# Kernel tuning notes

Hardware: AMD Instinct MI355X
Metric: run time of the kernel (lower is better)

## Reference

```python
import jax, jax.numpy as jnp
import numpy as np
from jax.scipy.linalg import solve_triangular

B, T, S, L, R, H = 64, 100, 32, 128, 16, 256

def bmv(A, v):
    return jnp.einsum('...ij,...j->...i', A, v)

def mT(A):
    return jnp.swapaxes(A, -1, -2)

def tri_inv_mT(chol):
    # Psi = inv(chol).T (upper triangular); chol is batched lower-triangular
    r = chol.shape[-1]
    I = jnp.broadcast_to(jnp.eye(r, dtype=chol.dtype), chol.shape)
    return mT(solve_triangular(chol, I, lower=True))

def chol_bmv_solve(Psi, v):
    # (chol chol^T)^{-1} v, using Psi = inv(chol)^T -> A^{-1} = Psi Psi^T
    return bmv(Psi, bmv(mT(Psi), v))

def filter_step_0(m_0, k0, K0, P_p_diag, w_p, w_f):
    # K0: (B,L,R); w_p: (S,B,L); w_f: (S,B,R)
    r = K0.shape[-1]
    z_p_c = jnp.sqrt(P_p_diag) * w_p
    m_p = jnp.broadcast_to(m_0, K0.shape[:1] + m_0.shape)  # (B,L)
    h = (1.0 / P_p_diag) * m_p + k0
    P_p_K = P_p_diag[None, :, None] * K0                    # (B,L,R)
    M = jnp.eye(r, dtype=K0.dtype) + mT(K0) @ P_p_K
    Psi = tri_inv_mT(jnp.linalg.cholesky(M))
    m = P_p_diag * h - bmv(P_p_K, chol_bmv_solve(Psi, bmv(mT(P_p_K), h)))
    v_1 = bmv(mT(K0), z_p_c) + w_f
    z = m + z_p_c - bmv(K0, chol_bmv_solve(Psi, v_1))
    return z, m

def predict_step(m_theta, Q_diag, w1, w2):
    # m_theta: (B,L,S) dynamics-mean particles
    s = m_theta.shape[-1]
    m_p = m_theta.mean(-1)                                   # (B,L)
    M_c = (m_theta - m_p[..., None]) * (1.0 / np.sqrt(s))    # (B,L,S)
    McT_Qinv = mT(M_c) * (1.0 / Q_diag)
    Psi_p = tri_inv_mT(jnp.linalg.cholesky(jnp.eye(s, dtype=m_theta.dtype) + McT_Qinv @ M_c))
    u1 = m_p / Q_diag
    u2 = (1.0 / Q_diag) * bmv(M_c, bmv(Psi_p, bmv(mT(Psi_p), bmv(mT(M_c), u1))))
    h_p = u1 - u2                                            # P_p^{-1} m_p (Woodbury)
    z_p_c = bmv(M_c, w1) + jnp.sqrt(Q_diag) * w2             # (S,B,L)
    return z_p_c, m_p, h_p, M_c

def update_step(z_p_c, h_p, k_t, K_t, w_f, M_c_p, Q_diag):
    r = K_t.shape[-1]
    Q_sqrt = jnp.sqrt(Q_diag)
    h = h_p + k_t
    K_M = mT(K_t) @ M_c_p                                    # (B,R,S)
    K_Q = mT(K_t) * Q_sqrt
    KPK = K_M @ mT(K_M) + K_Q @ mT(K_Q)                      # K^T P_p K
    Psi = tri_inv_mT(jnp.linalg.cholesky(jnp.eye(r, dtype=K_t.dtype) + KPK))
    P_p = lambda v: bmv(M_c_p, bmv(mT(M_c_p), v)) + Q_diag * v
    u1 = P_p(h)
    trip = bmv(K_t, bmv(Psi, bmv(mT(Psi), bmv(mT(K_t), u1))))
    m = u1 - P_p(trip)                                       # P_f h via Woodbury
    v_1 = bmv(mT(K_t), z_p_c) + w_f
    z = m + z_p_c - bmv(K_t, chol_bmv_solve(Psi, v_1))
    return m, z

def forward(k, K, m_0, P_p_diag, Q_diag, W1, W2, w_p0, w_f0, w_p1_seq, w_p2_seq, w_f_seq):
    mean_fn = lambda z: z + jnp.tanh(z @ W1) @ W2            # nonlinear dynamics mean
    k_tm = jnp.moveaxis(k, 1, 0)                              # (T,B,L)
    K_tm = jnp.moveaxis(K, 1, 0)                              # (T,B,L,R)
    z0, _ = filter_step_0(m_0, k_tm[0], K_tm[0], P_p_diag, w_p0, w_f0)

    def step(z_prev, inp):
        kt, Kt, w1, w2, wf = inp
        m_theta = jnp.moveaxis(mean_fn(z_prev), 0, -1)        # (B,L,S)
        z_p_c, m_p, h_p, M_c = predict_step(m_theta, Q_diag, w1, w2)
        m_f, z_f = update_step(z_p_c, h_p, kt, Kt, wf, M_c, Q_diag)
        return z_f, z_f

    _, zs = jax.lax.scan(step, z0, (k_tm[1:], K_tm[1:], w_p1_seq, w_p2_seq, w_f_seq))
    return jnp.concatenate([z0[None], zs], axis=0)            # (T,S,B,L)

def setup_inputs() -> dict:
    key = jax.random.key(0)
    ks = jax.random.split(key, 12)
    return {
        'k': 0.5 * jax.random.normal(ks[0], (B, T, L), jnp.float32),
        'K': 0.2 * jax.random.normal(ks[1], (B, T, L, R), jnp.float32),
        'm_0': jax.random.normal(ks[2], (L,), jnp.float32),
        'P_p_diag': jax.random.uniform(ks[3], (L,), jnp.float32, 0.5, 1.5),
        'Q_diag': jax.random.uniform(ks[4], (L,), jnp.float32, 0.5, 1.5),
        'W1': 0.02 * jax.random.normal(ks[5], (L, H), jnp.float32),
        'W2': 0.02 * jax.random.normal(ks[6], (H, L), jnp.float32),
        'w_p0': jax.random.normal(ks[7], (S, B, L), jnp.float32),
        'w_f0': jax.random.normal(ks[8], (S, B, R), jnp.float32),
        'w_p1_seq': jax.random.normal(ks[9], (T - 1, S, B, S), jnp.float32),
        'w_p2_seq': jax.random.normal(ks[10], (T - 1, S, B, L), jnp.float32),
        'w_f_seq': jax.random.normal(ks[11], (T - 1, S, B, R), jnp.float32),
    }

def reference(k, K, m_0, P_p_diag, Q_diag, W1, W2, w_p0, w_f0, w_p1_seq, w_p2_seq, w_f_seq):
    return forward(k, K, m_0, P_p_diag, Q_diag, W1, W2, w_p0, w_f0, w_p1_seq, w_p2_seq, w_f_seq)
```

## Files before the change

kernel.cpp:

```cpp
#include <hip/hip_runtime.h>
#include <math.h>

#define B_ 64
#define T_ 100
#define S_ 32
#define L_ 128
#define R_ 16
#define H_ 256

__device__ __forceinline__ float dot4(float4 a, float4 b) {
  return a.x*b.x + a.y*b.y + a.z*b.z + a.w*b.w;
}
__device__ __forceinline__ void wave_fence() {
  asm volatile("s_waitcnt lgkmcnt(0)" ::: "memory");
  __builtin_amdgcn_wave_barrier();
}

__device__ __forceinline__ void chol16_inv(int lane, float (*C2)[17], float (*G)[17], float* rd) {
  float row[16];
  #pragma unroll
  for (int c = 0; c < 16; ++c) row[c] = (lane < 16) ? C2[lane][c] : 0.0f;
  float rdg = 0.0f;
  #pragma unroll
  for (int j = 0; j < 16; ++j) {
    float dsq = __shfl(row[j], j);
    float d = sqrtf(dsq);
    float inv = 1.0f / d;
    float cij = row[j] * inv;
    if (lane == j) { cij = d; rdg = inv; }
    row[j] = cij;
    float upd = (lane > j) ? (cij * inv) : 0.0f;
    #pragma unroll
    for (int c = j + 1; c < 16; ++c) {
      float cjc = __shfl(row[c], j);
      row[c] -= upd * cjc;
    }
  }
  if (lane < 16) {
    #pragma unroll
    for (int c = 0; c < 16; ++c) C2[lane][c] = row[c];
    rd[lane] = rdg;
  }
  wave_fence();
  if (lane < 16) {
    const int c = lane;
    float g[16];
    #pragma unroll
    for (int i = 0; i < 16; ++i) {
      float a = (i == c) ? 1.0f : 0.0f;
      #pragma unroll
      for (int j2 = 0; j2 < 16; ++j2) if (j2 < i) a -= C2[i][j2] * g[j2];
      g[i] = a * rd[i];
    }
    #pragma unroll
    for (int i = 0; i < 16; ++i) G[i][c] = (i >= c) ? g[i] : 0.0f;
  }
  wave_fence();
}

__device__ __forceinline__ void chol32_solve(int lane, float (*C)[33], float* rd32,
                                             const float* t1, float* xb) {
  float row[32];
  #pragma unroll
  for (int c = 0; c < 32; ++c) row[c] = (lane < 32) ? C[lane][c] : 0.0f;
  float rdg = 0.0f;
  #pragma unroll
  for (int j = 0; j < 32; ++j) {
    float dsq = __shfl(row[j], j);
    float d = sqrtf(dsq);
    float inv = 1.0f / d;
    float cij = row[j] * inv;
    if (lane == j) { cij = d; rdg = inv; }
    row[j] = cij;
    float upd = (lane > j) ? (cij * inv) : 0.0f;
    #pragma unroll
    for (int c = j + 1; c < 32; ++c) {
      float cjc = __shfl(row[c], j);
      row[c] -= upd * cjc;
    }
  }
  float acc = (lane < 32) ? t1[lane] : 0.0f;
  #pragma unroll
  for (int j = 0; j < 32; ++j) {
    float xj = __shfl(acc, j) * __shfl(rdg, j);
    if (lane == j) acc = xj;
    else if (lane > j) acc -= row[j] * xj;
  }
  if (lane < 32) {
    #pragma unroll
    for (int c = 0; c < 32; ++c) C[lane][c] = row[c];
    rd32[lane] = rdg;
  }
  wave_fence();
  float acc2 = acc;
  #pragma unroll
  for (int j = 31; j >= 0; --j) {
    if (lane == j) xb[j] = acc2 * rdg;
    wave_fence();
    float xj = xb[j];
    if (lane < j) acc2 -= C[j][lane] * xj;
  }
}

__global__ __launch_bounds__(512) void filter_kernel(
    const float* __restrict__ kg,
    const float* __restrict__ Kg,
    const float* __restrict__ m0g,
    const float* __restrict__ Ppg,
    const float* __restrict__ Qg,
    const float* __restrict__ wp0,
    const float* __restrict__ wf0,
    const float* __restrict__ wp1s,
    const float* __restrict__ wp2s,
    const float* __restrict__ wfs,
    const float* __restrict__ W1,
    const float* __restrict__ W2,
    float* __restrict__ out)
{
  const int b = blockIdx.x;
  const int tid = threadIdx.x;

  __shared__ float zc[S_][132];
  __shared__ float Ab[S_][264];
  __shared__ float Mc[S_][132];
  __shared__ float zp[S_][132];
  __shared__ float KtT[R_][132];
  __shared__ float w1b[S_][36];
  __shared__ float wfb[S_][20];
  __shared__ float C32m[32][33];
  __shared__ float C2m[16][17];
  __shared__ float Gm[16][17];
  __shared__ float KMm[16][36];
  __shared__ float v1b[S_][20];
  __shared__ float yb[S_][20];
  __shared__ float xv[S_][20];
  __shared__ float red[32][17];
  __shared__ float mp[L_], u1[L_], hv[L_], uu[L_], mv[L_], trp[L_], ktv[L_];
  __shared__ float Qv[L_], iQ[L_], sQ[L_], Ppv[L_], sPp[L_], m0v[L_];
  __shared__ float t1v[32], tPh[32], xbuf[32], rd32[32];
  __shared__ float ttv[16], ssv[16], rd16[16], y2v[16];

  if (tid < L_) {
    float q = Qg[tid];  Qv[tid] = q;  iQ[tid] = 1.0f / q;  sQ[tid] = sqrtf(q);
    float p = Ppg[tid]; Ppv[tid] = p; sPp[tid] = sqrtf(p);
    m0v[tid] = m0g[tid];
  }
  __syncthreads();

  {
    {
      const float* Ksrc = Kg + (size_t)b * T_ * L_ * R_;
      float4 v = *(const float4*)(Ksrc + tid * 4);
      int l = (tid * 4) >> 4, r = (tid * 4) & 15;
      KtT[r+0][l] = v.x; KtT[r+1][l] = v.y; KtT[r+2][l] = v.z; KtT[r+3][l] = v.w;
    }
    for (int e = tid; e < S_ * L_ / 4; e += 512) {
      int s = e >> 5, l = (e & 31) * 4;
      float4 w = *(const float4*)(wp0 + ((size_t)s * B_ + b) * L_ + l);
      float4 p = *(const float4*)&sPp[l];
      *(float4*)&zp[s][l] = make_float4(w.x*p.x, w.y*p.y, w.z*p.z, w.w*p.w);
    }
    { int s = tid >> 4, r = tid & 15;
      wfb[s][r] = wf0[((size_t)s * B_ + b) * R_ + r]; }
    __syncthreads();

    if (tid < 256) {
      int r1 = tid >> 4, r2 = tid & 15;
      if (r1 <= r2) {
        float acc = (r1 == r2) ? 1.0f : 0.0f;
        for (int lc = 0; lc < 32; ++lc) {
          float4 a = *(const float4*)&KtT[r1][lc*4];
          float4 c = *(const float4*)&KtT[r2][lc*4];
          float4 p = *(const float4*)&Ppv[lc*4];
          acc += a.x*c.x*p.x + a.y*c.y*p.y + a.z*c.z*p.z + a.w*c.w*p.w;
        }
        C2m[r1][r2] = acc; C2m[r2][r1] = acc;
      }
      if (tid < 128) hv[tid] = m0v[tid] / Ppv[tid] + kg[(size_t)b * T_ * L_ + tid];
    } else {
      int q2 = tid - 256, s = q2 >> 3, r = (q2 & 7) * 2;
      float a0 = wfb[s][r], a1 = wfb[s][r+1];
      for (int lc = 0; lc < 32; ++lc) {
        float4 zz = *(const float4*)&zp[s][lc*4];
        float4 ka = *(const float4*)&KtT[r][lc*4];
        float4 kb = *(const float4*)&KtT[r+1][lc*4];
        a0 += dot4(zz, ka); a1 += dot4(zz, kb);
      }
      v1b[s][r] = a0; v1b[s][r+1] = a1;
    }
    __syncthreads();
    if (tid < 64) chol16_inv(tid, C2m, Gm, rd16);
    __syncthreads();
    {
      int r = tid & 15, g = tid >> 4;
      float4 a = *(const float4*)&KtT[r][g*4];
      float4 p = *(const float4*)&Ppv[g*4];
      float4 h4 = *(const float4*)&hv[g*4];
      red[g][r] = a.x*p.x*h4.x + a.y*p.y*h4.y + a.z*p.z*h4.z + a.w*p.w*h4.w;
    }
    { int s = tid >> 4, r = tid & 15;
      float a = 0;
      #pragma unroll
      for (int j = 0; j < 16; ++j) a += Gm[r][j] * v1b[s][j];
      yb[s][r] = a; }
    __syncthreads();
    {
      int s = tid >> 4, r = tid & 15;
      float a = 0;
      #pragma unroll
      for (int j = 0; j < 16; ++j) a += Gm[j][r] * yb[s][j];
      xv[s][r] = a; }
    if (tid < 64) {
      if (tid < 16) { float a = 0;
        #pragma unroll
        for (int g = 0; g < 32; ++g) a += red[g][tid];
        ttv[tid] = a; }
      wave_fence();
      if (tid < 16) { float a = 0;
        #pragma unroll
        for (int j = 0; j < 16; ++j) a += Gm[tid][j] * ttv[j];
        y2v[tid] = a; }
      wave_fence();
      if (tid < 16) { float a = 0;
        #pragma unroll
        for (int j = 0; j < 16; ++j) a += Gm[j][tid] * y2v[j];
        ssv[tid] = a; }
    }
    __syncthreads();
    if (tid < 128) {
      float a = hv[tid];
      #pragma unroll
      for (int r = 0; r < 16; ++r) a -= KtT[r][tid] * ssv[r];
      mv[tid] = Ppv[tid] * a;
    }
    __syncthreads();
    {
      int s = tid >> 4, l0 = (tid & 15) * 8;
      float acc[8] = {0,0,0,0,0,0,0,0};
      #pragma unroll
      for (int r = 0; r < 16; ++r) {
        float xr = xv[s][r];
        float4 k1 = *(const float4*)&KtT[r][l0];
        float4 k2 = *(const float4*)&KtT[r][l0+4];
        acc[0] += k1.x*xr; acc[1] += k1.y*xr; acc[2] += k1.z*xr; acc[3] += k1.w*xr;
        acc[4] += k2.x*xr; acc[5] += k2.y*xr; acc[6] += k2.z*xr; acc[7] += k2.w*xr;
      }
      float4 o1, o2;
      o1.x = mv[l0+0] + zp[s][l0+0] - acc[0]; o1.y = mv[l0+1] + zp[s][l0+1] - acc[1];
      o1.z = mv[l0+2] + zp[s][l0+2] - acc[2]; o1.w = mv[l0+3] + zp[s][l0+3] - acc[3];
      o2.x = mv[l0+4] + zp[s][l0+4] - acc[4]; o2.y = mv[l0+5] + zp[s][l0+5] - acc[5];
      o2.z = mv[l0+6] + zp[s][l0+6] - acc[6]; o2.w = mv[l0+7] + zp[s][l0+7] - acc[7];
      *(float4*)&zc[s][l0] = o1; *(float4*)&zc[s][l0+4] = o2;
      float* orow = out + ((size_t)s * B_ + b) * L_ + l0;
      *(float4*)orow = o1; *(float4*)(orow + 4) = o2;
    }
    __syncthreads();
  }

  for (int t = 1; t < T_; ++t) {
    {
      const float* Ksrc = Kg + ((size_t)b * T_ + t) * L_ * R_;
      float4 v = *(const float4*)(Ksrc + tid * 4);
      int l = (tid * 4) >> 4, r = (tid * 4) & 15;
      KtT[r+0][l] = v.x; KtT[r+1][l] = v.y; KtT[r+2][l] = v.z; KtT[r+3][l] = v.w;
    }
    if (tid < 128) ktv[tid] = kg[((size_t)b * T_ + t) * L_ + tid];
    { int s = tid >> 4, r = tid & 15;
      wfb[s][r] = wfs[(((size_t)(t-1) * S_ + s) * B_ + b) * R_ + r]; }
    { int e = tid * 2, s = e >> 5, j = e & 31;
      float2 v = *(const float2*)(wp1s + (((size_t)(t-1) * S_ + s) * B_ + b) * S_ + j);
      w1b[s][j] = v.x; w1b[s][j+1] = v.y; }

    {
      int s = tid & 31, h0 = (tid >> 5) * 16;
      float acc[16] = {0,0,0,0,0,0,0,0,0,0,0,0,0,0,0,0};
      for (int lc = 0; lc < 32; ++lc) {
        float4 z4 = *(const float4*)&zc[s][lc*4];
        float zv[4] = {z4.x, z4.y, z4.z, z4.w};
        #pragma unroll
        for (int q = 0; q < 4; ++q) {
          const float* wrow = W1 + (lc*4 + q) * H_ + h0;
          float4 wa = *(const float4*)(wrow);
          float4 wb = *(const float4*)(wrow + 4);
          float4 wc = *(const float4*)(wrow + 8);
          float4 wd = *(const float4*)(wrow + 12);
          float zq = zv[q];
          acc[0]  += zq*wa.x; acc[1]  += zq*wa.y; acc[2]  += zq*wa.z; acc[3]  += zq*wa.w;
          acc[4]  += zq*wb.x; acc[5]  += zq*wb.y; acc[6]  += zq*wb.z; acc[7]  += zq*wb.w;
          acc[8]  += zq*wc.x; acc[9]  += zq*wc.y; acc[10] += zq*wc.z; acc[11] += zq*wc.w;
          acc[12] += zq*wd.x; acc[13] += zq*wd.y; acc[14] += zq*wd.z; acc[15] += zq*wd.w;
        }
      }
      #pragma unroll
      for (int j = 0; j < 16; ++j) Ab[s][h0 + j] = tanhf(acc[j]);
    }
    __syncthreads();
    {
      int s = tid & 31, l0 = (tid >> 5) * 8;
      float acc[8] = {0,0,0,0,0,0,0,0};
      for (int hc = 0; hc < 64; ++hc) {
        float4 a4 = *(const float4*)&Ab[s][hc*4];
        float av[4] = {a4.x, a4.y, a4.z, a4.w};
        #pragma unroll
        for (int q = 0; q < 4; ++q) {
          const float* wrow = W2 + (hc*4 + q) * L_ + l0;
          float4 wa = *(const float4*)(wrow);
          float4 wb = *(const float4*)(wrow + 4);
          float aq = av[q];
          acc[0] += aq*wa.x; acc[1] += aq*wa.y; acc[2] += aq*wa.z; acc[3] += aq*wa.w;
          acc[4] += aq*wb.x; acc[5] += aq*wb.y; acc[6] += aq*wb.z; acc[7] += aq*wb.w;
        }
      }
      #pragma unroll
      for (int j = 0; j < 8; ++j) Mc[s][l0 + j] = zc[s][l0 + j] + acc[j];
    }
    __syncthreads();
    if (tid < 128) {
      float m = 0;
      #pragma unroll 8
      for (int s = 0; s < 32; ++s) m += Mc[s][tid];
      m *= (1.0f / 32.0f);
      mp[tid] = m; u1[tid] = m * iQ[tid];
    }
    __syncthreads();
    for (int e = tid; e < S_ * L_; e += 512) {
      int s = e >> 7, l = e & 127;
      float v = (Mc[s][l] - mp[l]) * 0.17677669529663687f;
      Mc[s][l] = v; Ab[s][l] = v * iQ[l];
    }
    __syncthreads();
    for (int e = tid; e < 1024; e += 512) {
      int s1 = e >> 5, s2 = e & 31;
      if (s1 <= s2) {
        float acc = (s1 == s2) ? 1.0f : 0.0f;
        for (int lc = 0; lc < 32; ++lc) {
          float4 a = *(const float4*)&Ab[s1][lc*4];
          float4 c = *(const float4*)&Mc[s2][lc*4];
          acc += dot4(a, c);
        }
        C32m[s1][s2] = acc; C32m[s2][s1] = acc;
      }
    }
    { int s = tid >> 4, r = tid & 15;
      float acc = 0;
      for (int lc = 0; lc < 32; ++lc) {
        float4 kk = *(const float4*)&KtT[r][lc*4];
        float4 mm = *(const float4*)&Mc[s][lc*4];
        acc += dot4(kk, mm);
      }
      KMm[r][s] = acc; }
    { int s = tid >> 4, g = tid & 15, l0 = g * 8;
      float4 m1 = *(const float4*)&Mc[s][l0];
      float4 m2 = *(const float4*)&Mc[s][l0+4];
      float4 a1 = *(const float4*)&u1[l0];
      float4 a2 = *(const float4*)&u1[l0+4];
      red[s][g] = dot4(m1, a1) + dot4(m2, a2); }
    { int s = tid >> 4, l0 = (tid & 15) * 8;
      float acc[8] = {0,0,0,0,0,0,0,0};
      for (int j = 0; j < 32; ++j) {
        float wj = w1b[s][j];
        float4 m1 = *(const float4*)&Mc[j][l0];
        float4 m2 = *(const float4*)&Mc[j][l0+4];
        acc[0] += m1.x*wj; acc[1] += m1.y*wj; acc[2] += m1.z*wj; acc[3] += m1.w*wj;
        acc[4] += m2.x*wj; acc[5] += m2.y*wj; acc[6] += m2.z*wj; acc[7] += m2.w*wj;
      }
      const float* w2src = wp2s + (((size_t)(t-1) * S_ + s) * B_ + b) * L_ + l0;
      float4 wa = *(const float4*)(w2src);
      float4 wb2 = *(const float4*)(w2src + 4);
      float4 q1 = *(const float4*)&sQ[l0];
      float4 q2 = *(const float4*)&sQ[l0+4];
      *(float4*)&zp[s][l0]   = make_float4(acc[0]+q1.x*wa.x,  acc[1]+q1.y*wa.y,
                                           acc[2]+q1.z*wa.z,  acc[3]+q1.w*wa.w);
      *(float4*)&zp[s][l0+4] = make_float4(acc[4]+q2.x*wb2.x, acc[5]+q2.y*wb2.y,
                                           acc[6]+q2.z*wb2.z, acc[7]+q2.w*wb2.w); }
    __syncthreads();
    if (tid < 256) {
      int r1 = tid >> 4, r2 = tid & 15;
      if (r1 <= r2) {
        float acc = (r1 == r2) ? 1.0f : 0.0f;
        #pragma unroll
        for (int sc2 = 0; sc2 < 8; ++sc2) {
          float4 a = *(const float4*)&KMm[r1][sc2*4];
          float4 c = *(const float4*)&KMm[r2][sc2*4];
          acc += dot4(a, c);
        }
        for (int lc = 0; lc < 32; ++lc) {
          float4 a = *(const float4*)&KtT[r1][lc*4];
          float4 c = *(const float4*)&KtT[r2][lc*4];
          float4 q = *(const float4*)&Qv[lc*4];
          acc += a.x*c.x*q.x + a.y*c.y*q.y + a.z*c.z*q.z + a.w*c.w*q.w;
        }
        C2m[r1][r2] = acc; C2m[r2][r1] = acc;
      }
      if (tid < 32) { float a = 0;
        #pragma unroll
        for (int g = 0; g < 16; ++g) a += red[tid][g];
        t1v[tid] = a; }
    } else {
      int q2 = tid - 256, s = q2 >> 3, r = (q2 & 7) * 2;
      float a0 = wfb[s][r], a1 = wfb[s][r+1];
      for (int lc = 0; lc < 32; ++lc) {
        float4 zz = *(const float4*)&zp[s][lc*4];
        float4 ka = *(const float4*)&KtT[r][lc*4];
        float4 kb = *(const float4*)&KtT[r+1][lc*4];
        a0 += dot4(zz, ka); a1 += dot4(zz, kb);
      }
      v1b[s][r] = a0; v1b[s][r+1] = a1;
    }
    __syncthreads();
    if (tid < 64) chol32_solve(tid, C32m, rd32, t1v, xbuf);
    else if (tid < 128) chol16_inv(tid - 64, C2m, Gm, rd16);
    __syncthreads();
    { int s = tid >> 4, r = tid & 15;
      float a = 0;
      #pragma unroll
      for (int j = 0; j < 16; ++j) a += Gm[r][j] * v1b[s][j];
      yb[s][r] = a; }
    if (tid < 128) {
      float a = u1[tid];
      #pragma unroll 8
      for (int s = 0; s < 32; ++s) a -= Ab[s][tid] * xbuf[s];
      hv[tid] = a + ktv[tid];
    }
    __syncthreads();
    { int s = tid >> 4, r = tid & 15;
      float a = 0;
      #pragma unroll
      for (int j = 0; j < 16; ++j) a += Gm[j][r] * yb[s][j];
      xv[s][r] = a; }
    { int s = tid >> 4, g = tid & 15, l0 = g * 8;
      float4 m1 = *(const float4*)&Mc[s][l0];
      float4 m2 = *(const float4*)&Mc[s][l0+4];
      float4 h1 = *(const float4*)&hv[l0];
      float4 h2 = *(const float4*)&hv[l0+4];
      red[s][g] = dot4(m1, h1) + dot4(m2, h2); }
    __syncthreads();
    if (tid < 32) { float a = 0;
      #pragma unroll
      for (int g = 0; g < 16; ++g) a += red[tid][g];
      tPh[tid] = a; }
    __syncthreads();
    if (tid < 128) {
      float a = Qv[tid] * hv[tid];
      #pragma unroll 8
      for (int s = 0; s < 32; ++s) a += Mc[s][tid] * tPh[s];
      uu[tid] = a;
    }
    __syncthreads();
    { int r = tid & 15, g = tid >> 4;
      float4 a = *(const float4*)&KtT[r][g*4];
      float4 u4 = *(const float4*)&uu[g*4];
      red[g][r] = dot4(a, u4); }
    __syncthreads();
    if (tid < 64) {
      if (tid < 16) { float a = 0;
        #pragma unroll
        for (int g = 0; g < 32; ++g) a += red[g][tid];
        ttv[tid] = a; }
      wave_fence();
      if (tid < 16) { float a = 0;
        #pragma unroll
        for (int j = 0; j < 16; ++j) a += Gm[tid][j] * ttv[j];
        y2v[tid] = a; }
      wave_fence();
      if (tid < 16) { float a = 0;
        #pragma unroll
        for (int j = 0; j < 16; ++j) a += Gm[j][tid] * y2v[j];
        ssv[tid] = a; }
    }
    __syncthreads();
    if (tid < 128) {
      float a = 0;
      #pragma unroll
      for (int r = 0; r < 16; ++r) a += KtT[r][tid] * ssv[r];
      trp[tid] = a;
    }
    __syncthreads();
    { int s = tid >> 4, g = tid & 15, l0 = g * 8;
      float4 m1 = *(const float4*)&Mc[s][l0];
      float4 m2 = *(const float4*)&Mc[s][l0+4];
      float4 h1 = *(const float4*)&trp[l0];
      float4 h2 = *(const float4*)&trp[l0+4];
      red[s][g] = dot4(m1, h1) + dot4(m2, h2); }
    __syncthreads();
    if (tid < 32) { float a = 0;
      #pragma unroll
      for (int g = 0; g < 16; ++g) a += red[tid][g];
      tPh[tid] = a; }
    __syncthreads();
    if (tid < 128) {
      float a = uu[tid] - Qv[tid] * trp[tid];
      #pragma unroll 8
      for (int s = 0; s < 32; ++s) a -= Mc[s][tid] * tPh[s];
      mv[tid] = a;
    }
    __syncthreads();
    {
      int s = tid >> 4, l0 = (tid & 15) * 8;
      float acc[8] = {0,0,0,0,0,0,0,0};
      #pragma unroll
      for (int r = 0; r < 16; ++r) {
        float xr = xv[s][r];
        float4 k1 = *(const float4*)&KtT[r][l0];
        float4 k2 = *(const float4*)&KtT[r][l0+4];
        acc[0] += k1.x*xr; acc[1] += k1.y*xr; acc[2] += k1.z*xr; acc[3] += k1.w*xr;
        acc[4] += k2.x*xr; acc[5] += k2.y*xr; acc[6] += k2.z*xr; acc[7] += k2.w*xr;
      }
      float4 o1, o2;
      o1.x = mv[l0+0] + zp[s][l0+0] - acc[0]; o1.y = mv[l0+1] + zp[s][l0+1] - acc[1];
      o1.z = mv[l0+2] + zp[s][l0+2] - acc[2]; o1.w = mv[l0+3] + zp[s][l0+3] - acc[3];
      o2.x = mv[l0+4] + zp[s][l0+4] - acc[4]; o2.y = mv[l0+5] + zp[s][l0+5] - acc[5];
      o2.z = mv[l0+6] + zp[s][l0+6] - acc[6]; o2.w = mv[l0+7] + zp[s][l0+7] - acc[7];
      *(float4*)&zc[s][l0] = o1; *(float4*)&zc[s][l0+4] = o2;
      float* orow = out + (((size_t)t * S_ + s) * B_ + b) * L_ + l0;
      *(float4*)orow = o1; *(float4*)(orow + 4) = o2;
    }
    __syncthreads();
  }
}

extern "C" void kernel_launch(void* const* d_in, const int* in_sizes, int n_in,
                              void* d_out, int out_size, void* d_ws, size_t ws_size,
                              hipStream_t stream) {
  const float* kg  = (const float*)d_in[0];
  const float* Kg  = (const float*)d_in[1];
  const float* m0  = (const float*)d_in[2];
  const float* Pp  = (const float*)d_in[3];
  const float* Qd  = (const float*)d_in[4];
  const float* W1  = (const float*)d_in[5];
  const float* W2  = (const float*)d_in[6];
  const float* wp0 = (const float*)d_in[7];
  const float* wf0 = (const float*)d_in[8];
  const float* wp1 = (const float*)d_in[9];
  const float* wp2 = (const float*)d_in[10];
  const float* wfs = (const float*)d_in[11];
  float* outp = (float*)d_out;
  (void)d_ws; (void)ws_size;

  filter_kernel<<<B_, 512, 0, stream>>>(kg, Kg, m0, Pp, Qd, wp0, wf0,
                                        wp1, wp2, wfs, W1, W2, outp);
}
```

Baseline: 8.575 ms.

## Double block to 1024 threads and collapse serial update chain into one wave

Each block now runs 1024 threads. The MLP and prediction phases are re-split so each thread does less work. The long chain of small reductions in the update step (hv, tPh, uu, ttv, ssv, trp, mv), which used many block-wide barriers, now runs inside a single 64-lane wave using shuffles and wave fences, while other waves compute the Kalman-gain correction to zp in parallel. The 32x32 back-substitution now uses register shuffles instead of per-step LDS writes and fences, and a transposed Mc copy is added for column access. The aim is to cut __syncthreads count and latency on this serial per-timestep path. The cost is more LDS use, more register pressure under the 1024-thread launch bound, and most threads sitting idle during the single-wave section.

```diff
diff --git a/kernel.cpp b/kernel.cpp
--- a/kernel.cpp
+++ b/kernel.cpp
@@ -58,8 +58,8 @@
   wave_fence();
 }
 
-__device__ __forceinline__ void chol32_solve(int lane, float (*C)[33], float* rd32,
-                                             const float* t1, float* xb) {
+__device__ __forceinline__ void chol32_fs(int lane, float (*C)[33],
+                                          const float* t1, float* xb) {
   float row[32];
   #pragma unroll
   for (int c = 0; c < 32; ++c) row[c] = (lane < 32) ? C[lane][c] : 0.0f;
@@ -89,20 +89,24 @@
   if (lane < 32) {
     #pragma unroll
     for (int c = 0; c < 32; ++c) C[lane][c] = row[c];
-    rd32[lane] = rdg;
   }
   wave_fence();
+  float colT[32];
+  #pragma unroll
+  for (int j = 0; j < 32; ++j) colT[j] = (lane < 32) ? C[j][lane] : 0.0f;
   float acc2 = acc;
+  float xi = 0.0f;
   #pragma unroll
   for (int j = 31; j >= 0; --j) {
-    if (lane == j) xb[j] = acc2 * rdg;
-    wave_fence();
-    float xj = xb[j];
-    if (lane < j) acc2 -= C[j][lane] * xj;
-  }
+    float xj = __shfl(acc2, j) * __shfl(rdg, j);
+    if (lane == j) xi = xj;
+    if (lane < j) acc2 -= colT[j] * xj;
+  }
+  if (lane < 32) xb[lane] = xi;
+  wave_fence();
 }
 
-__global__ __launch_bounds__(512) void filter_kernel(
+__global__ __launch_bounds__(1024) void filter_kernel(
     const float* __restrict__ kg,
     const float* __restrict__ Kg,
     const float* __restrict__ m0g,
@@ -123,6 +127,7 @@
   __shared__ float zc[S_][132];
   __shared__ float Ab[S_][264];
   __shared__ float Mc[S_][132];
+  __shared__ float McT[L_][33];
   __shared__ float zp[S_][132];
   __shared__ float KtT[R_][132];
   __shared__ float w1b[S_][36];
@@ -133,11 +138,11 @@
   __shared__ float KMm[16][36];
   __shared__ float v1b[S_][20];
   __shared__ float yb[S_][20];
-  __shared__ float xv[S_][20];
+  __shared__ float xvb[S_][20];
   __shared__ float red[32][17];
   __shared__ float mp[L_], u1[L_], hv[L_], uu[L_], mv[L_], trp[L_], ktv[L_];
   __shared__ float Qv[L_], iQ[L_], sQ[L_], Ppv[L_], sPp[L_], m0v[L_];
-  __shared__ float t1v[32], tPh[32], xbuf[32], rd32[32];
+  __shared__ float t1v[32], tPh[32], xbuf[32];
   __shared__ float ttv[16], ssv[16], rd16[16], y2v[16];
 
   if (tid < L_) {
@@ -148,19 +153,19 @@
   __syncthreads();
 
   {
-    {
+    if (tid < 512) {
       const float* Ksrc = Kg + (size_t)b * T_ * L_ * R_;
       float4 v = *(const float4*)(Ksrc + tid * 4);
       int l = (tid * 4) >> 4, r = (tid * 4) & 15;
       KtT[r+0][l] = v.x; KtT[r+1][l] = v.y; KtT[r+2][l] = v.z; KtT[r+3][l] = v.w;
     }
-    for (int e = tid; e < S_ * L_ / 4; e += 512) {
-      int s = e >> 5, l = (e & 31) * 4;
+    {
+      int s = tid >> 5, l = (tid & 31) * 4;
       float4 w = *(const float4*)(wp0 + ((size_t)s * B_ + b) * L_ + l);
       float4 p = *(const float4*)&sPp[l];
       *(float4*)&zp[s][l] = make_float4(w.x*p.x, w.y*p.y, w.z*p.z, w.w*p.w);
     }
-    { int s = tid >> 4, r = tid & 15;
+    if (tid < 512) { int s = tid >> 4, r = tid & 15;
       wfb[s][r] = wf0[((size_t)s * B_ + b) * R_ + r]; }
     __syncthreads();
 
@@ -177,7 +182,7 @@
         C2m[r1][r2] = acc; C2m[r2][r1] = acc;
       }
       if (tid < 128) hv[tid] = m0v[tid] / Ppv[tid] + kg[(size_t)b * T_ * L_ + tid];
-    } else {
+    } else if (tid < 512) {
       int q2 = tid - 256, s = q2 >> 3, r = (q2 & 7) * 2;
       float a0 = wfb[s][r], a1 = wfb[s][r+1];
       for (int lc = 0; lc < 32; ++lc) {
@@ -191,25 +196,24 @@
     __syncthreads();
     if (tid < 64) chol16_inv(tid, C2m, Gm, rd16);
     __syncthreads();
-    {
-      int r = tid & 15, g = tid >> 4;
-      float4 a = *(const float4*)&KtT[r][g*4];
-      float4 p = *(const float4*)&Ppv[g*4];
-      float4 h4 = *(const float4*)&hv[g*4];
-      red[g][r] = a.x*p.x*h4.x + a.y*p.y*h4.y + a.z*p.z*h4.z + a.w*p.w*h4.w;
-    }
-    { int s = tid >> 4, r = tid & 15;
+    if (tid < 512) {
+      { int r = tid & 15, g = tid >> 4;
+        float4 a = *(const float4*)&KtT[r][g*4];
+        float4 p = *(const float4*)&Ppv[g*4];
+        float4 h4 = *(const float4*)&hv[g*4];
+        red[g][r] = a.x*p.x*h4.x + a.y*p.y*h4.y + a.z*p.z*h4.z + a.w*p.w*h4.w; }
+      { int s = tid >> 4, r = tid & 15;
+        float a = 0;
+        #pragma unroll
+        for (int j = 0; j < 16; ++j) a += Gm[r][j] * v1b[s][j];
+        yb[s][r] = a; }
+    }
+    __syncthreads();
+    if (tid < 512) { int s = tid >> 4, r = tid & 15;
       float a = 0;
       #pragma unroll
-      for (int j = 0; j < 16; ++j) a += Gm[r][j] * v1b[s][j];
-      yb[s][r] = a; }
-    __syncthreads();
-    {
-      int s = tid >> 4, r = tid & 15;
-      float a = 0;
-      #pragma unroll
       for (int j = 0; j < 16; ++j) a += Gm[j][r] * yb[s][j];
-      xv[s][r] = a; }
+      xvb[s][r] = a; }
     if (tid < 64) {
       if (tid < 16) { float a = 0;
         #pragma unroll
@@ -234,12 +238,12 @@
       mv[tid] = Ppv[tid] * a;
     }
     __syncthreads();
-    {
+    if (tid < 512) {
       int s = tid >> 4, l0 = (tid & 15) * 8;
       float acc[8] = {0,0,0,0,0,0,0,0};
       #pragma unroll
       for (int r = 0; r < 16; ++r) {
-        float xr = xv[s][r];
+        float xr = xvb[s][r];
         float4 k1 = *(const float4*)&KtT[r][l0];
         float4 k2 = *(const float4*)&KtT[r][l0+4];
         acc[0] += k1.x*xr; acc[1] += k1.y*xr; acc[2] += k1.z*xr; acc[3] += k1.w*xr;
@@ -258,61 +262,56 @@
   }
 
   for (int t = 1; t < T_; ++t) {
-    {
+    if (tid < 512) {
       const float* Ksrc = Kg + ((size_t)b * T_ + t) * L_ * R_;
       float4 v = *(const float4*)(Ksrc + tid * 4);
       int l = (tid * 4) >> 4, r = (tid * 4) & 15;
       KtT[r+0][l] = v.x; KtT[r+1][l] = v.y; KtT[r+2][l] = v.z; KtT[r+3][l] = v.w;
-    }
-    if (tid < 128) ktv[tid] = kg[((size_t)b * T_ + t) * L_ + tid];
-    { int s = tid >> 4, r = tid & 15;
-      wfb[s][r] = wfs[(((size_t)(t-1) * S_ + s) * B_ + b) * R_ + r]; }
-    { int e = tid * 2, s = e >> 5, j = e & 31;
+      int s = tid >> 4, rr = tid & 15;
+      wfb[s][rr] = wfs[(((size_t)(t-1) * S_ + s) * B_ + b) * R_ + rr];
+      if (tid < 128) ktv[tid] = kg[((size_t)b * T_ + t) * L_ + tid];
+    } else {
+      int e = (tid - 512) * 2, s = e >> 5, j = e & 31;
       float2 v = *(const float2*)(wp1s + (((size_t)(t-1) * S_ + s) * B_ + b) * S_ + j);
-      w1b[s][j] = v.x; w1b[s][j+1] = v.y; }
+      w1b[s][j] = v.x; w1b[s][j+1] = v.y;
+    }
 
     {
-      int s = tid & 31, h0 = (tid >> 5) * 16;
-      float acc[16] = {0,0,0,0,0,0,0,0,0,0,0,0,0,0,0,0};
+      int s = tid >> 5, h0 = (tid & 31) * 8;
+      float acc[8] = {0,0,0,0,0,0,0,0};
       for (int lc = 0; lc < 32; ++lc) {
         float4 z4 = *(const float4*)&zc[s][lc*4];
+        const float* wbase = W1 + (size_t)(lc*4) * H_ + h0;
         float zv[4] = {z4.x, z4.y, z4.z, z4.w};
         #pragma unroll
         for (int q = 0; q < 4; ++q) {
-          const float* wrow = W1 + (lc*4 + q) * H_ + h0;
-          float4 wa = *(const float4*)(wrow);
-          float4 wb = *(const float4*)(wrow + 4);
-          float4 wc = *(const float4*)(wrow + 8);
-          float4 wd = *(const float4*)(wrow + 12);
+          float4 wa = *(const float4*)(wbase + q*H_);
+          float4 wb = *(const float4*)(wbase + q*H_ + 4);
           float zq = zv[q];
-          acc[0]  += zq*wa.x; acc[1]  += zq*wa.y; acc[2]  += zq*wa.z; acc[3]  += zq*wa.w;
-          acc[4]  += zq*wb.x; acc[5]  += zq*wb.y; acc[6]  += zq*wb.z; acc[7]  += zq*wb.w;
-          acc[8]  += zq*wc.x; acc[9]  += zq*wc.y; acc[10] += zq*wc.z; acc[11] += zq*wc.w;
-          acc[12] += zq*wd.x; acc[13] += zq*wd.y; acc[14] += zq*wd.z; acc[15] += zq*wd.w;
-        }
-      }
-      #pragma unroll
-      for (int j = 0; j < 16; ++j) Ab[s][h0 + j] = tanhf(acc[j]);
+          acc[0] += zq*wa.x; acc[1] += zq*wa.y; acc[2] += zq*wa.z; acc[3] += zq*wa.w;
+          acc[4] += zq*wb.x; acc[5] += zq*wb.y; acc[6] += zq*wb.z; acc[7] += zq*wb.w;
+        }
+      }
+      #pragma unroll
+      for (int j = 0; j < 8; ++j) Ab[s][h0 + j] = tanhf(acc[j]);
     }
     __syncthreads();
     {
-      int s = tid & 31, l0 = (tid >> 5) * 8;
-      float acc[8] = {0,0,0,0,0,0,0,0};
+      int s = tid >> 5, l0 = (tid & 31) * 4;
+      float acc[4] = {0,0,0,0};
       for (int hc = 0; hc < 64; ++hc) {
         float4 a4 = *(const float4*)&Ab[s][hc*4];
+        const float* wbase = W2 + (size_t)(hc*4) * L_ + l0;
         float av[4] = {a4.x, a4.y, a4.z, a4.w};
         #pragma unroll
         for (int q = 0; q < 4; ++q) {
-          const float* wrow = W2 + (hc*4 + q) * L_ + l0;
-          float4 wa = *(const float4*)(wrow);
-          float4 wb = *(const float4*)(wrow + 4);
+          float4 w = *(const float4*)(wbase + q*L_);
           float aq = av[q];
-          acc[0] += aq*wa.x; acc[1] += aq*wa.y; acc[2] += aq*wa.z; acc[3] += aq*wa.w;
-          acc[4] += aq*wb.x; acc[5] += aq*wb.y; acc[6] += aq*wb.z; acc[7] += aq*wb.w;
-        }
-      }
-      #pragma unroll
-      for (int j = 0; j < 8; ++j) Mc[s][l0 + j] = zc[s][l0 + j] + acc[j];
+          acc[0] += aq*w.x; acc[1] += aq*w.y; acc[2] += aq*w.z; acc[3] += aq*w.w;
+        }
+      }
+      float4 z4 = *(const float4*)&zc[s][l0];
+      *(float4*)&Mc[s][l0] = make_float4(z4.x+acc[0], z4.y+acc[1], z4.z+acc[2], z4.w+acc[3]);
     }
     __syncthreads();
     if (tid < 128) {
@@ -323,56 +322,58 @@
       mp[tid] = m; u1[tid] = m * iQ[tid];
     }
     __syncthreads();
-    for (int e = tid; e < S_ * L_; e += 512) {
-      int s = e >> 7, l = e & 127;
-      float v = (Mc[s][l] - mp[l]) * 0.17677669529663687f;
-      Mc[s][l] = v; Ab[s][l] = v * iQ[l];
-    }
-    __syncthreads();
-    for (int e = tid; e < 1024; e += 512) {
-      int s1 = e >> 5, s2 = e & 31;
-      if (s1 <= s2) {
-        float acc = (s1 == s2) ? 1.0f : 0.0f;
+    {
+      int s = tid >> 5, l0 = (tid & 31) * 4;
+      float4 m4 = *(const float4*)&Mc[s][l0];
+      float4 p4 = *(const float4*)&mp[l0];
+      float4 q4 = *(const float4*)&iQ[l0];
+      const float cs = 0.17677669529663687f;
+      float4 v4 = make_float4((m4.x-p4.x)*cs, (m4.y-p4.y)*cs, (m4.z-p4.z)*cs, (m4.w-p4.w)*cs);
+      *(float4*)&Mc[s][l0] = v4;
+      *(float4*)&Ab[s][l0] = make_float4(v4.x*q4.x, v4.y*q4.y, v4.z*q4.z, v4.w*q4.w);
+      McT[l0+0][s] = v4.x; McT[l0+1][s] = v4.y; McT[l0+2][s] = v4.z; McT[l0+3][s] = v4.w;
+    }
+    __syncthreads();
+    {
+      { int s1 = tid >> 5, s2 = tid & 31;
+        if (s1 <= s2) {
+          float acc = (s1 == s2) ? 1.0f : 0.0f;
+          for (int lc = 0; lc < 32; ++lc) {
+            float4 a = *(const float4*)&Ab[s1][lc*4];
+            float4 c = *(const float4*)&Mc[s2][lc*4];
+            acc += dot4(a, c);
+          }
+          C32m[s1][s2] = acc; C32m[s2][s1] = acc;
+        } }
+      if (tid < 512) { int r = tid >> 5, s = tid & 31;
+        float acc = 0;
         for (int lc = 0; lc < 32; ++lc) {
-          float4 a = *(const float4*)&Ab[s1][lc*4];
-          float4 c = *(const float4*)&Mc[s2][lc*4];
-          acc += dot4(a, c);
-        }
-        C32m[s1][s2] = acc; C32m[s2][s1] = acc;
-      }
-    }
-    { int s = tid >> 4, r = tid & 15;
-      float acc = 0;
-      for (int lc = 0; lc < 32; ++lc) {
-        float4 kk = *(const float4*)&KtT[r][lc*4];
-        float4 mm = *(const float4*)&Mc[s][lc*4];
-        acc += dot4(kk, mm);
-      }
-      KMm[r][s] = acc; }
-    { int s = tid >> 4, g = tid & 15, l0 = g * 8;
-      float4 m1 = *(const float4*)&Mc[s][l0];
-      float4 m2 = *(const float4*)&Mc[s][l0+4];
-      float4 a1 = *(const float4*)&u1[l0];
-      float4 a2 = *(const float4*)&u1[l0+4];
-      red[s][g] = dot4(m1, a1) + dot4(m2, a2); }
-    { int s = tid >> 4, l0 = (tid & 15) * 8;
-      float acc[8] = {0,0,0,0,0,0,0,0};
-      for (int j = 0; j < 32; ++j) {
-        float wj = w1b[s][j];
-        float4 m1 = *(const float4*)&Mc[j][l0];
-        float4 m2 = *(const float4*)&Mc[j][l0+4];
-        acc[0] += m1.x*wj; acc[1] += m1.y*wj; acc[2] += m1.z*wj; acc[3] += m1.w*wj;
-        acc[4] += m2.x*wj; acc[5] += m2.y*wj; acc[6] += m2.z*wj; acc[7] += m2.w*wj;
-      }
-      const float* w2src = wp2s + (((size_t)(t-1) * S_ + s) * B_ + b) * L_ + l0;
-      float4 wa = *(const float4*)(w2src);
-      float4 wb2 = *(const float4*)(w2src + 4);
-      float4 q1 = *(const float4*)&sQ[l0];
-      float4 q2 = *(const float4*)&sQ[l0+4];
-      *(float4*)&zp[s][l0]   = make_float4(acc[0]+q1.x*wa.x,  acc[1]+q1.y*wa.y,
-                                           acc[2]+q1.z*wa.z,  acc[3]+q1.w*wa.w);
-      *(float4*)&zp[s][l0+4] = make_float4(acc[4]+q2.x*wb2.x, acc[5]+q2.y*wb2.y,
-                                           acc[6]+q2.z*wb2.z, acc[7]+q2.w*wb2.w); }
+          float4 kk = *(const float4*)&KtT[r][lc*4];
+          float4 mm = *(const float4*)&Mc[s][lc*4];
+          acc += dot4(kk, mm);
+        }
+        KMm[r][s] = acc;
+      } else { int g = tid - 512, s = g >> 4, seg = g & 15;
+        float4 m1 = *(const float4*)&Mc[s][seg*8];
+        float4 m2 = *(const float4*)&Mc[s][seg*8+4];
+        float4 a1 = *(const float4*)&u1[seg*8];
+        float4 a2 = *(const float4*)&u1[seg*8+4];
+        red[s][seg] = dot4(m1, a1) + dot4(m2, a2);
+      }
+      {
+        int s = tid >> 5, l0 = (tid & 31) * 4;
+        float a0=0, a1=0, a2=0, a3=0;
+        for (int j = 0; j < 32; ++j) {
+          float wj = w1b[s][j];
+          float4 m4 = *(const float4*)&Mc[j][l0];
+          a0 += m4.x*wj; a1 += m4.y*wj; a2 += m4.z*wj; a3 += m4.w*wj;
+        }
+        const float* w2src = wp2s + (((size_t)(t-1) * S_ + s) * B_ + b) * L_ + l0;
+        float4 wv = *(const float4*)(w2src);
+        float4 q4 = *(const float4*)&sQ[l0];
+        *(float4*)&zp[s][l0] = make_float4(a0+q4.x*wv.x, a1+q4.y*wv.y, a2+q4.z*wv.z, a3+q4.w*wv.w);
+      }
+    }
     __syncthreads();
     if (tid < 256) {
       int r1 = tid >> 4, r2 = tid & 15;
@@ -392,128 +393,144 @@
         }
         C2m[r1][r2] = acc; C2m[r2][r1] = acc;
       }
-      if (tid < 32) { float a = 0;
-        #pragma unroll
-        for (int g = 0; g < 16; ++g) a += red[tid][g];
-        t1v[tid] = a; }
-    } else {
-      int q2 = tid - 256, s = q2 >> 3, r = (q2 & 7) * 2;
-      float a0 = wfb[s][r], a1 = wfb[s][r+1];
+    } else if (tid < 288) {
+      int s = tid - 256;
+      float a = 0;
+      #pragma unroll
+      for (int g = 0; g < 16; ++g) a += red[s][g];
+      t1v[s] = a;
+    } else if (tid >= 512) {
+      int g = tid - 512, s = g >> 4, r = g & 15;
+      float a = wfb[s][r];
       for (int lc = 0; lc < 32; ++lc) {
         float4 zz = *(const float4*)&zp[s][lc*4];
-        float4 ka = *(const float4*)&KtT[r][lc*4];
-        float4 kb = *(const float4*)&KtT[r+1][lc*4];
-        a0 += dot4(zz, ka); a1 += dot4(zz, kb);
-      }
-      v1b[s][r] = a0; v1b[s][r+1] = a1;
-    }
-    __syncthreads();
-    if (tid < 64) chol32_solve(tid, C32m, rd32, t1v, xbuf);
+        float4 kk = *(const float4*)&KtT[r][lc*4];
+        a += dot4(zz, kk);
+      }
+      v1b[s][r] = a;
+    }
+    __syncthreads();
+    if (tid < 64) chol32_fs(tid, C32m, t1v, xbuf);
     else if (tid < 128) chol16_inv(tid - 64, C2m, Gm, rd16);
     __syncthreads();
-    { int s = tid >> 4, r = tid & 15;
-      float a = 0;
-      #pragma unroll
-      for (int j = 0; j < 16; ++j) a += Gm[r][j] * v1b[s][j];
-      yb[s][r] = a; }
-    if (tid < 128) {
-      float a = u1[tid];
-      #pragma unroll 8
-      for (int s = 0; s < 32; ++s) a -= Ab[s][tid] * xbuf[s];
-      hv[tid] = a + ktv[tid];
-    }
-    __syncthreads();
-    { int s = tid >> 4, r = tid & 15;
-      float a = 0;
-      #pragma unroll
-      for (int j = 0; j < 16; ++j) a += Gm[j][r] * yb[s][j];
-      xv[s][r] = a; }
-    { int s = tid >> 4, g = tid & 15, l0 = g * 8;
-      float4 m1 = *(const float4*)&Mc[s][l0];
-      float4 m2 = *(const float4*)&Mc[s][l0+4];
-      float4 h1 = *(const float4*)&hv[l0];
-      float4 h2 = *(const float4*)&hv[l0+4];
-      red[s][g] = dot4(m1, h1) + dot4(m2, h2); }
-    __syncthreads();
-    if (tid < 32) { float a = 0;
-      #pragma unroll
-      for (int g = 0; g < 16; ++g) a += red[tid][g];
-      tPh[tid] = a; }
-    __syncthreads();
-    if (tid < 128) {
-      float a = Qv[tid] * hv[tid];
-      #pragma unroll 8
-      for (int s = 0; s < 32; ++s) a += Mc[s][tid] * tPh[s];
-      uu[tid] = a;
-    }
-    __syncthreads();
-    { int r = tid & 15, g = tid >> 4;
-      float4 a = *(const float4*)&KtT[r][g*4];
-      float4 u4 = *(const float4*)&uu[g*4];
-      red[g][r] = dot4(a, u4); }
-    __syncthreads();
     if (tid < 64) {
-      if (tid < 16) { float a = 0;
-        #pragma unroll
-        for (int g = 0; g < 32; ++g) a += red[g][tid];
-        ttv[tid] = a; }
-      wave_fence();
-      if (tid < 16) { float a = 0;
-        #pragma unroll
-        for (int j = 0; j < 16; ++j) a += Gm[tid][j] * ttv[j];
-        y2v[tid] = a; }
-      wave_fence();
-      if (tid < 16) { float a = 0;
-        #pragma unroll
-        for (int j = 0; j < 16; ++j) a += Gm[j][tid] * y2v[j];
-        ssv[tid] = a; }
-    }
-    __syncthreads();
-    if (tid < 128) {
-      float a = 0;
-      #pragma unroll
-      for (int r = 0; r < 16; ++r) a += KtT[r][tid] * ssv[r];
-      trp[tid] = a;
-    }
-    __syncthreads();
-    { int s = tid >> 4, g = tid & 15, l0 = g * 8;
-      float4 m1 = *(const float4*)&Mc[s][l0];
-      float4 m2 = *(const float4*)&Mc[s][l0+4];
-      float4 h1 = *(const float4*)&trp[l0];
-      float4 h2 = *(const float4*)&trp[l0+4];
-      red[s][g] = dot4(m1, h1) + dot4(m2, h2); }
-    __syncthreads();
-    if (tid < 32) { float a = 0;
-      #pragma unroll
-      for (int g = 0; g < 16; ++g) a += red[tid][g];
-      tPh[tid] = a; }
-    __syncthreads();
-    if (tid < 128) {
-      float a = uu[tid] - Qv[tid] * trp[tid];
-      #pragma unroll 8
-      for (int s = 0; s < 32; ++s) a -= Mc[s][tid] * tPh[s];
-      mv[tid] = a;
+      const int ln = tid;
+      const int l0 = ln, l1 = ln + 64;
+      float a0 = 0.f, a1 = 0.f;
+      for (int s = 0; s < 32; ++s) {
+        float xs = xbuf[s];
+        a0 += McT[l0][s] * xs; a1 += McT[l1][s] * xs;
+      }
+      hv[l0] = u1[l0] + ktv[l0] - iQ[l0] * a0;
+      hv[l1] = u1[l1] + ktv[l1] - iQ[l1] * a1;
+      wave_fence();
+      {
+        int s = ln & 31, hb = (ln >> 5) * 64;
+        float p = 0;
+        #pragma unroll
+        for (int l = 0; l < 64; l += 4) {
+          float4 m4 = *(const float4*)&Mc[s][hb+l];
+          float4 h4 = *(const float4*)&hv[hb+l];
+          p += dot4(m4, h4);
+        }
+        p += __shfl_xor(p, 32);
+        if (ln < 32) tPh[s] = p;
+      }
+      wave_fence();
+      a0 = 0.f; a1 = 0.f;
+      for (int s = 0; s < 32; ++s) {
+        float ts = tPh[s];
+        a0 += McT[l0][s] * ts; a1 += McT[l1][s] * ts;
+      }
+      uu[l0] = Qv[l0]*hv[l0] + a0;
+      uu[l1] = Qv[l1]*hv[l1] + a1;
+      wave_fence();
+      float ttr;
+      { int r = ln & 15, qd = ln >> 4;
+        float p = 0;
+        #pragma unroll
+        for (int l = 0; l < 32; l += 4) {
+          float4 k4 = *(const float4*)&KtT[r][qd*32+l];
+          float4 u4 = *(const float4*)&uu[qd*32+l];
+          p += dot4(k4, u4);
+        }
+        p += __shfl_xor(p, 16);
+        p += __shfl_xor(p, 32);
+        ttr = p;
+      }
+      { int r = ln & 15;
+        float y2 = 0;
+        #pragma unroll
+        for (int j = 0; j < 16; ++j) y2 += Gm[r][j] * __shfl(ttr, j);
+        float ssr = 0;
+        #pragma unroll
+        for (int j = 0; j < 16; ++j) ssr += Gm[j][r] * __shfl(y2, j);
+        if (ln < 16) ssv[r] = ssr;
+      }
+      wave_fence();
+      a0 = 0.f; a1 = 0.f;
+      #pragma unroll
+      for (int r = 0; r < 16; ++r) {
+        float sr = ssv[r];
+        a0 += KtT[r][l0] * sr; a1 += KtT[r][l1] * sr;
+      }
+      trp[l0] = a0; trp[l1] = a1;
+      wave_fence();
+      {
+        int s = ln & 31, hb = (ln >> 5) * 64;
+        float p = 0;
+        #pragma unroll
+        for (int l = 0; l < 64; l += 4) {
+          float4 m4 = *(const float4*)&Mc[s][hb+l];
+          float4 h4 = *(const float4*)&trp[hb+l];
+          p += dot4(m4, h4);
+        }
+        p += __shfl_xor(p, 32);
+        if (ln < 32) tPh[s] = p;
+      }
+      wave_fence();
+      a0 = 0.f; a1 = 0.f;
+      for (int s = 0; s < 32; ++s) {
+        float ts = tPh[s];
+        a0 += McT[l0][s] * ts; a1 += McT[l1][s] * ts;
+      }
+      mv[l0] = uu[l0] - Qv[l0]*trp[l0] - a0;
+      mv[l1] = uu[l1] - Qv[l1]*trp[l1] - a1;
+    } else if (tid < 576) {
+      int g = tid - 64;
+      int s = g >> 4, r = g & 15;
+      int sb = (g & 63) & 48;
+      float yv = 0;
+      #pragma unroll
+      for (int j = 0; j < 16; ++j) yv += Gm[r][j] * v1b[s][j];
+      float xr_ = 0;
+      #pragma unroll
+      for (int j = 0; j < 16; ++j) xr_ += Gm[j][r] * __shfl(yv, sb + j);
+      float xl[16];
+      #pragma unroll
+      for (int j = 0; j < 16; ++j) xl[j] = __shfl(xr_, sb + j);
+      int lb = r * 8;
+      float acc[8] = {0,0,0,0,0,0,0,0};
+      #pragma unroll
+      for (int r2 = 0; r2 < 16; ++r2) {
+        float xr = xl[r2];
+        #pragma unroll
+        for (int i = 0; i < 8; ++i) acc[i] += KtT[r2][lb+i] * xr;
+      }
+      float4 z1 = *(const float4*)&zp[s][lb];
+      float4 z2 = *(const float4*)&zp[s][lb+4];
+      z1.x -= acc[0]; z1.y -= acc[1]; z1.z -= acc[2]; z1.w -= acc[3];
+      z2.x -= acc[4]; z2.y -= acc[5]; z2.z -= acc[6]; z2.w -= acc[7];
+      *(float4*)&zp[s][lb] = z1; *(float4*)&zp[s][lb+4] = z2;
     }
     __syncthreads();
     {
-      int s = tid >> 4, l0 = (tid & 15) * 8;
-      float acc[8] = {0,0,0,0,0,0,0,0};
-      #pragma unroll
-      for (int r = 0; r < 16; ++r) {
-        float xr = xv[s][r];
-        float4 k1 = *(const float4*)&KtT[r][l0];
-        float4 k2 = *(const float4*)&KtT[r][l0+4];
-        acc[0] += k1.x*xr; acc[1] += k1.y*xr; acc[2] += k1.z*xr; acc[3] += k1.w*xr;
-        acc[4] += k2.x*xr; acc[5] += k2.y*xr; acc[6] += k2.z*xr; acc[7] += k2.w*xr;
-      }
-      float4 o1, o2;
-      o1.x = mv[l0+0] + zp[s][l0+0] - acc[0]; o1.y = mv[l0+1] + zp[s][l0+1] - acc[1];
-      o1.z = mv[l0+2] + zp[s][l0+2] - acc[2]; o1.w = mv[l0+3] + zp[s][l0+3] - acc[3];
-      o2.x = mv[l0+4] + zp[s][l0+4] - acc[4]; o2.y = mv[l0+5] + zp[s][l0+5] - acc[5];
-      o2.z = mv[l0+6] + zp[s][l0+6] - acc[6]; o2.w = mv[l0+7] + zp[s][l0+7] - acc[7];
-      *(float4*)&zc[s][l0] = o1; *(float4*)&zc[s][l0+4] = o2;
-      float* orow = out + (((size_t)t * S_ + s) * B_ + b) * L_ + l0;
-      *(float4*)orow = o1; *(float4*)(orow + 4) = o2;
+      int s = tid >> 5, l0 = (tid & 31) * 4;
+      float4 z4 = *(const float4*)&zp[s][l0];
+      float4 m4 = *(const float4*)&mv[l0];
+      z4.x += m4.x; z4.y += m4.y; z4.z += m4.z; z4.w += m4.w;
+      *(float4*)&zc[s][l0] = z4;
+      *(float4*)(out + (((size_t)t * S_ + s) * B_ + b) * L_ + l0) = z4;
     }
     __syncthreads();
   }
@@ -537,6 +554,6 @@
   float* outp = (float*)d_out;
   (void)d_ws; (void)ws_size;
 
-  filter_kernel<<<B_, 512, 0, stream>>>(kg, Kg, m0, Pp, Qd, wp0, wf0,
-                                        wp1, wp2, wfs, W1, W2, outp);
+  filter_kernel<<<B_, 1024, 0, stream>>>(kg, Kg, m0, Pp, Qd, wp0, wf0,
+                                         wp1, wp2, wfs, W1, W2, outp);
 }
```

After: 8.585 ms. No clear change (+0.1%).
